# Performance work log

Hardware: AMD Instinct MI355X
Metric: run time of the kernel (lower is better)

Reference implementation:

```python
import jax, jax.numpy as jnp
import numpy as np

HEADS = 16
DIM_HEAD = 64
SCALE = DIM_HEAD ** -0.5


def setup_inputs() -> dict:
    key = jax.random.key(0)
    k1, k2, k3, k4 = jax.random.split(key, 4)
    b, n, dim = 2, 2048, 1024
    inner = HEADS * DIM_HEAD  # 1024
    return {
        "x": jax.random.normal(k1, (b, n, dim), dtype=jnp.float32),
        "x1": jax.random.normal(k2, (b, n, dim), dtype=jnp.float32),
        "W_qkv": jax.random.normal(k3, (dim, inner * 3), dtype=jnp.float32) * (dim ** -0.5),
        "W_out": jax.random.normal(k4, (inner, dim), dtype=jnp.float32) * (inner ** -0.5),
        "b_out": jnp.zeros((dim,), dtype=jnp.float32),
    }


def _split_heads(t):
    b, n, hd = t.shape
    return t.reshape(b, n, HEADS, DIM_HEAD).transpose(0, 2, 1, 3)  # b h n d


def _merge_heads(t):
    b, h, n, d = t.shape
    return t.transpose(0, 2, 1, 3).reshape(b, n, h * d)


def reference(x, x1, W_qkv, W_out, b_out):
    qkv = jnp.split(x @ W_qkv, 3, axis=-1)
    qkv1 = jnp.split(x1 @ W_qkv, 3, axis=-1)
    q, k, v = map(_split_heads, qkv)
    q1, k1, v1 = map(_split_heads, qkv1)

    # cross attention: x queries attend to x1 keys/values, and vice versa
    attn = jax.nn.softmax(jnp.einsum('bhnd,bhmd->bhnm', q, k1) * SCALE, axis=-1)
    attn1 = jax.nn.softmax(jnp.einsum('bhnd,bhmd->bhnm', q1, k) * SCALE, axis=-1)
    out = _merge_heads(jnp.einsum('bhnm,bhmd->bhnd', attn, v1))
    out1 = _merge_heads(jnp.einsum('bhnm,bhmd->bhnd', attn1, v))

    out = out @ W_out + b_out
    out1 = out1 @ W_out + b_out
    return out, out1
```

## Files before the change

kernel.cpp:

```cpp
#include <hip/hip_runtime.h>
#include <hip/hip_bf16.h>


typedef __attribute__((ext_vector_type(8))) short short8;
typedef __attribute__((ext_vector_type(4))) float f32x4;

#define MFMA_BF16(a, b, c) __builtin_amdgcn_mfma_f32_16x16x32_bf16((a), (b), (c), 0, 0, 0)

__device__ __forceinline__ ushort f2bf(float f) {
    __hip_bfloat16 h = __float2bfloat16(f);
    return *reinterpret_cast<ushort*>(&h);
}

__device__ __forceinline__ void gload_lds16(const void* g, void* l) {
    __builtin_amdgcn_global_load_lds(
        (const __attribute__((address_space(1))) void*)g,
        (__attribute__((address_space(3))) void*)l, 16, 0, 0);
}

__global__ __launch_bounds__(256) void cvt_k(const float* __restrict__ in,
                                             ushort* __restrict__ out, int n) {
    const int i = (blockIdx.x * 256 + threadIdx.x) * 4;
    if (i >= n) return;
    float4 v = *(const float4*)(in + i);
    ushort4 o;
    o.x = f2bf(v.x); o.y = f2bf(v.y); o.z = f2bf(v.z); o.w = f2bf(v.w);
    *(ushort4*)(out + i) = o;
}

__global__ __launch_bounds__(256) void transpose_cvt(const float* __restrict__ in,
                                                     ushort* __restrict__ out,
                                                     int R, int C) {
    __shared__ ushort tile[32][33];
    const int c0 = blockIdx.x * 32, r0 = blockIdx.y * 32;
    const int tx = threadIdx.x, ty = threadIdx.y;
#pragma unroll
    for (int i = 0; i < 4; ++i)
        tile[ty * 4 + i][tx] = f2bf(in[(size_t)(r0 + ty * 4 + i) * C + c0 + tx]);
    __syncthreads();
#pragma unroll
    for (int i = 0; i < 4; ++i)
        out[(size_t)(c0 + ty * 4 + i) * R + r0 + tx] = tile[tx][ty * 4 + i];
}

__global__ __launch_bounds__(256) void qkv_gemm(const ushort* __restrict__ xb,
                                                const ushort* __restrict__ wt,
                                                ushort* __restrict__ qb,
                                                ushort* __restrict__ kb,
                                                ushort* __restrict__ vb) {
    __shared__ __align__(16) ushort As[128][40];
    __shared__ __align__(16) ushort Bs[128][40];

    const int n0 = blockIdx.x * 128;
    const int m0 = blockIdx.y * 128;
    const int t = threadIdx.x;
    const int lane = t & 63, w = t >> 6;
    const int wm = (w >> 1) * 64, wn = (w & 1) * 64;
    const int l16 = lane & 15, lq = lane >> 4;
    const int r = t >> 1, kc = (t & 1) * 16;

    f32x4 acc[4][4] = {};

    for (int k0 = 0; k0 < 1024; k0 += 32) {
        __syncthreads();
        {
            const ushort* p = xb + (size_t)(m0 + r) * 1024 + k0 + kc;
            short8 v0 = *(const short8*)p;
            short8 v1 = *(const short8*)(p + 8);
            *(short8*)&As[r][kc] = v0;
            *(short8*)&As[r][kc + 8] = v1;
            const ushort* q = wt + (size_t)(n0 + r) * 1024 + k0 + kc;
            short8 u0 = *(const short8*)q;
            short8 u1 = *(const short8*)(q + 8);
            *(short8*)&Bs[r][kc] = u0;
            *(short8*)&Bs[r][kc + 8] = u1;
        }
        __syncthreads();
        short8 a[4], b[4];
#pragma unroll
        for (int i = 0; i < 4; ++i) a[i] = *(const short8*)&As[wm + i * 16 + l16][lq * 8];
#pragma unroll
        for (int j = 0; j < 4; ++j) b[j] = *(const short8*)&Bs[wn + j * 16 + l16][lq * 8];
#pragma unroll
        for (int i = 0; i < 4; ++i)
#pragma unroll
            for (int j = 0; j < 4; ++j) acc[i][j] = MFMA_BF16(a[i], b[j], acc[i][j]);
    }

    const int which = (n0 >> 10);
    const float qscale = (which == 0) ? 0.125f : 1.0f;

#pragma unroll
    for (int i = 0; i < 4; ++i) {
#pragma unroll
        for (int jj = 0; jj < 4; ++jj) {
#pragma unroll
            for (int rr = 0; rr < 4; ++rr) {
                const int m = m0 + wm + i * 16 + lq * 4 + rr;
                const int nc = n0 + wn + jj * 16 + l16;
                const ushort bv = f2bf(acc[i][jj][rr] * qscale);
                const int s = m >> 12;
                const int mm = m & 4095;
                const int rem = nc & 1023;
                const int h = rem >> 6, d = rem & 63;
                const int sb = (s << 1) | (mm >> 11);
                const int pos = mm & 2047;
                const size_t bh = (size_t)(sb * 16 + h);
                if (which == 0)      qb[(bh * 2048 + pos) * 64 + d] = bv;
                else if (which == 1) kb[(bh * 2048 + pos) * 64 + d] = bv;
                else                 vb[(bh * 64 + d) * 2048 + pos] = bv;
            }
        }
    }
}

__global__ __launch_bounds__(256, 4) void attn_k(const ushort* __restrict__ qb,
                                                 const ushort* __restrict__ kb,
                                                 const ushort* __restrict__ vb,
                                                 ushort* __restrict__ ob) {
    __shared__ __align__(16) ushort Ks[2][4096];
    __shared__ __align__(16) ushort Vs[2][4096];
    __shared__ __align__(16) ushort Pt[4][1024];

    const int t = threadIdx.x, lane = t & 63, w = t >> 6;
    const int l16 = lane & 15, lq = lane >> 4;

    const int lid = blockIdx.x;
    const int xcd = lid & 7, kk = lid >> 3;
    const int qt = kk & 15;
    const int g = xcd + ((kk >> 4) << 3);
    const int h = g & 15, sb = g >> 4;
    const int s = sb >> 1, bb = sb & 1;
    const int kvsb = ((1 - s) << 1) | bb;
    const int q0 = qt * 128 + w * 32;

    const ushort* qp = qb + (size_t)(sb * 16 + h) * 2048 * 64;
    const char* kp = (const char*)(kb + (size_t)(kvsb * 16 + h) * 2048 * 64);
    const char* vp = (const char*)(vb + (size_t)(kvsb * 16 + h) * 64 * 2048);

    short8 aq[2][2];
#pragma unroll
    for (int u = 0; u < 2; ++u)
#pragma unroll
        for (int c = 0; c < 2; ++c)
            aq[u][c] = *(const short8*)(qp + (size_t)(q0 + u * 16 + l16) * 64 + c * 32 + lq * 8);

    short8 ones;
#pragma unroll
    for (int j = 0; j < 8; ++j) ones[j] = (short)0x3F80;

    f32x4 o_acc[2][4] = {};
    f32x4 l_acc[2] = {};

    const int swl = ((lane >> 3) & 7) << 4;
    auto stage = [&](int buf, int key0) {
#pragma unroll
        for (int i = 0; i < 2; ++i) {
            const int ch = w * 2 + i;
            const int off = ch * 1024 + lane * 16;
            gload_lds16(kp + (size_t)key0 * 128 + (off ^ swl),
                        (char*)&Ks[buf][0] + ch * 1024);
            const int rd = ch * 8 + (lane >> 3);
            const int cb = (lane & 7) * 16;
            gload_lds16(vp + (size_t)rd * 4096 + (size_t)key0 * 2 + (cb ^ swl),
                        (char*)&Vs[buf][0] + ch * 1024);
        }
    };

    stage(0, 0);
    __syncthreads();

    char* Pw = (char*)&Pt[w][0];

    for (int tt = 0; tt < 32; ++tt) {
        const int cur = tt & 1;
        if (tt < 31) stage(cur ^ 1, (tt + 1) * 64);

        const char* Kc = (const char*)&Ks[cur][0];
        const char* Vc = (const char*)&Vs[cur][0];

        f32x4 sc0[4] = {}, sc1[4] = {};
#pragma unroll
        for (int j = 0; j < 4; ++j) {
            const int row = j * 16 + l16;
            const int swr = (row & 7) << 4;
            short8 k0 = *(const short8*)(Kc + row * 128 + ((lq * 16) ^ swr));
            short8 k1 = *(const short8*)(Kc + row * 128 + ((64 + lq * 16) ^ swr));
            sc0[j] = MFMA_BF16(aq[0][0], k0, sc0[j]);
            sc0[j] = MFMA_BF16(aq[0][1], k1, sc0[j]);
            sc1[j] = MFMA_BF16(aq[1][0], k0, sc1[j]);
            sc1[j] = MFMA_BF16(aq[1][1], k1, sc1[j]);
        }

        short8 ap[2][2];
#pragma unroll
        for (int j = 0; j < 4; ++j)
#pragma unroll
            for (int r2 = 0; r2 < 4; ++r2) {
                const int row = lq * 4 + r2;
                *(ushort*)(Pw + row * 128 + ((j * 32 + l16 * 2) ^ ((row & 7) << 4))) =
                    f2bf(__expf(sc0[j][r2]));
            }
        asm volatile("s_waitcnt lgkmcnt(0)" ::: "memory");
        {
            const int swr = (l16 & 7) << 4;
            ap[0][0] = *(const short8*)(Pw + l16 * 128 + ((lq * 16) ^ swr));
            ap[0][1] = *(const short8*)(Pw + l16 * 128 + ((64 + lq * 16) ^ swr));
        }
        asm volatile("s_waitcnt lgkmcnt(0)" ::: "memory");
#pragma unroll
        for (int j = 0; j < 4; ++j)
#pragma unroll
            for (int r2 = 0; r2 < 4; ++r2) {
                const int row = lq * 4 + r2;
                *(ushort*)(Pw + row * 128 + ((j * 32 + l16 * 2) ^ ((row & 7) << 4))) =
                    f2bf(__expf(sc1[j][r2]));
            }
        asm volatile("s_waitcnt lgkmcnt(0)" ::: "memory");
        {
            const int swr = (l16 & 7) << 4;
            ap[1][0] = *(const short8*)(Pw + l16 * 128 + ((lq * 16) ^ swr));
            ap[1][1] = *(const short8*)(Pw + l16 * 128 + ((64 + lq * 16) ^ swr));
        }

        l_acc[0] = MFMA_BF16(ap[0][0], ones, l_acc[0]);
        l_acc[0] = MFMA_BF16(ap[0][1], ones, l_acc[0]);
        l_acc[1] = MFMA_BF16(ap[1][0], ones, l_acc[1]);
        l_acc[1] = MFMA_BF16(ap[1][1], ones, l_acc[1]);
#pragma unroll
        for (int dt = 0; dt < 4; ++dt) {
            const int row = dt * 16 + l16;
            const int swr = (row & 7) << 4;
            short8 v0 = *(const short8*)(Vc + row * 128 + ((lq * 16) ^ swr));
            short8 v1 = *(const short8*)(Vc + row * 128 + ((64 + lq * 16) ^ swr));
            o_acc[0][dt] = MFMA_BF16(ap[0][0], v0, o_acc[0][dt]);
            o_acc[0][dt] = MFMA_BF16(ap[0][1], v1, o_acc[0][dt]);
            o_acc[1][dt] = MFMA_BF16(ap[1][0], v0, o_acc[1][dt]);
            o_acc[1][dt] = MFMA_BF16(ap[1][1], v1, o_acc[1][dt]);
        }

        __syncthreads();
    }

#pragma unroll
    for (int u = 0; u < 2; ++u) {
        float inv[4];
#pragma unroll
        for (int r2 = 0; r2 < 4; ++r2) inv[r2] = 1.f / l_acc[u][r2];
#pragma unroll
        for (int dt = 0; dt < 4; ++dt)
#pragma unroll
            for (int r2 = 0; r2 < 4; ++r2)
                ob[(size_t)(sb * 2048 + q0 + u * 16 + lq * 4 + r2) * 1024 + h * 64 + dt * 16 + l16] =
                    f2bf(o_acc[u][dt][r2] * inv[r2]);
    }
}

__global__ __launch_bounds__(256) void out_gemm(const ushort* __restrict__ ob,
                                                const ushort* __restrict__ wot,
                                                const float* __restrict__ bias,
                                                float* __restrict__ out) {
    __shared__ __align__(16) ushort As[128][40];
    __shared__ __align__(16) ushort Bs[128][40];

    const int n0 = blockIdx.x * 128;
    const int m0 = blockIdx.y * 128;
    const int t = threadIdx.x;
    const int lane = t & 63, w = t >> 6;
    const int wm = (w >> 1) * 64, wn = (w & 1) * 64;
    const int l16 = lane & 15, lq = lane >> 4;
    const int r = t >> 1, kc = (t & 1) * 16;

    f32x4 acc[4][4] = {};

    for (int k0 = 0; k0 < 1024; k0 += 32) {
        __syncthreads();
        {
            const ushort* p = ob + (size_t)(m0 + r) * 1024 + k0 + kc;
            short8 v0 = *(const short8*)p;
            short8 v1 = *(const short8*)(p + 8);
            *(short8*)&As[r][kc] = v0;
            *(short8*)&As[r][kc + 8] = v1;
            const ushort* q = wot + (size_t)(n0 + r) * 1024 + k0 + kc;
            short8 u0 = *(const short8*)q;
            short8 u1 = *(const short8*)(q + 8);
            *(short8*)&Bs[r][kc] = u0;
            *(short8*)&Bs[r][kc + 8] = u1;
        }
        __syncthreads();
        short8 a[4], b[4];
#pragma unroll
        for (int i = 0; i < 4; ++i) a[i] = *(const short8*)&As[wm + i * 16 + l16][lq * 8];
#pragma unroll
        for (int j = 0; j < 4; ++j) b[j] = *(const short8*)&Bs[wn + j * 16 + l16][lq * 8];
#pragma unroll
        for (int i = 0; i < 4; ++i)
#pragma unroll
            for (int j = 0; j < 4; ++j) acc[i][j] = MFMA_BF16(a[i], b[j], acc[i][j]);
    }

    float biasf[4];
#pragma unroll
    for (int jj = 0; jj < 4; ++jj) biasf[jj] = bias[n0 + wn + jj * 16 + l16];

#pragma unroll
    for (int i = 0; i < 4; ++i)
#pragma unroll
        for (int jj = 0; jj < 4; ++jj)
#pragma unroll
            for (int rr = 0; rr < 4; ++rr) {
                const int m = m0 + wm + i * 16 + lq * 4 + rr;
                const int nc = n0 + wn + jj * 16 + l16;
                out[(size_t)m * 1024 + nc] = acc[i][jj][rr] + biasf[jj];
            }
}

extern "C" void kernel_launch(void* const* d_in, const int* in_sizes, int n_in,
                              void* d_out, int out_size, void* d_ws, size_t ws_size,
                              hipStream_t stream) {
    (void)out_size; (void)ws_size;
    const float *x = nullptr, *x1 = nullptr, *wqkv = nullptr, *wout = nullptr, *bias = nullptr;
    for (int i = 0; i < n_in; ++i) {
        const int sz = in_sizes[i];
        const float* p = (const float*)d_in[i];
        if (sz == 4194304)      { if (!x) x = p; else x1 = p; }
        else if (sz == 3145728) wqkv = p;
        else if (sz == 1048576) wout = p;
        else if (sz == 1024)    bias = p;
    }
    float* out = (float*)d_out;

    ushort* ws      = (ushort*)d_ws;
    ushort* wqkv_t  = ws;
    ushort* wout_t  = wqkv_t + 3072 * 1024;
    ushort* xb      = wout_t + 1024 * 1024;
    ushort* qbuf    = xb + 8388608;
    ushort* kbuf    = qbuf + 8388608;
    ushort* vbuf    = kbuf + 8388608;
    ushort* obuf    = xb;

    cvt_k<<<4096, 256, 0, stream>>>(x,  xb,           4194304);
    cvt_k<<<4096, 256, 0, stream>>>(x1, xb + 4194304, 4194304);
    transpose_cvt<<<dim3(96, 32), dim3(32, 8), 0, stream>>>(wqkv, wqkv_t, 1024, 3072);
    transpose_cvt<<<dim3(32, 32), dim3(32, 8), 0, stream>>>(wout, wout_t, 1024, 1024);
    qkv_gemm<<<dim3(24, 64), 256, 0, stream>>>(xb, wqkv_t, qbuf, kbuf, vbuf);
    attn_k<<<1024, 256, 0, stream>>>(qbuf, kbuf, vbuf, obuf);
    out_gemm<<<dim3(8, 64), 256, 0, stream>>>(obuf, wout_t, bias, out);
}
```

Measured before the change: 320.8 us.

## Use direct global-to-LDS loads with XOR swizzle and BK=64 in GEMMs

Both projection GEMMs now stage A and B tiles through global_load_lds 16-byte transfers into an XOR-swizzled LDS layout, and the K step doubles to 64. The goal is to skip the register round-trip for tile staging, avoid LDS bank conflicts, and halve the number of barriers per K sweep. The two input conversion launches are also merged into one kernel. In exchange, LDS use per block grows and there is still no double buffering, so load latency stays exposed between the barriers.

After: 306.6 us. 4.5% less time.

```diff
diff --git a/kernel.cpp b/kernel.cpp
--- a/kernel.cpp
+++ b/kernel.cpp
@@ -18,14 +18,17 @@
         (__attribute__((address_space(3))) void*)l, 16, 0, 0);
 }
 
-__global__ __launch_bounds__(256) void cvt_k(const float* __restrict__ in,
-                                             ushort* __restrict__ out, int n) {
-    const int i = (blockIdx.x * 256 + threadIdx.x) * 4;
-    if (i >= n) return;
-    float4 v = *(const float4*)(in + i);
+__global__ __launch_bounds__(256) void cvt2_k(const float* __restrict__ a,
+                                              const float* __restrict__ b,
+                                              ushort* __restrict__ out) {
+    const int idx = blockIdx.x * 256 + threadIdx.x;
+    const int half = 1048576;
+    const float* src = (idx < half) ? a : b;
+    const int i = (idx < half ? idx : idx - half) * 4;
+    float4 v = *(const float4*)(src + i);
     ushort4 o;
     o.x = f2bf(v.x); o.y = f2bf(v.y); o.z = f2bf(v.z); o.w = f2bf(v.w);
-    *(ushort4*)(out + i) = o;
+    *(ushort4*)(out + (size_t)idx * 4) = o;
 }
 
 __global__ __launch_bounds__(256) void transpose_cvt(const float* __restrict__ in,
@@ -48,8 +51,8 @@
                                                 ushort* __restrict__ qb,
                                                 ushort* __restrict__ kb,
                                                 ushort* __restrict__ vb) {
-    __shared__ __align__(16) ushort As[128][40];
-    __shared__ __align__(16) ushort Bs[128][40];
+    __shared__ __align__(16) ushort As[128 * 64];
+    __shared__ __align__(16) ushort Bs[128 * 64];
 
     const int n0 = blockIdx.x * 128;
     const int m0 = blockIdx.y * 128;
@@ -57,34 +60,44 @@
     const int lane = t & 63, w = t >> 6;
     const int wm = (w >> 1) * 64, wn = (w & 1) * 64;
     const int l16 = lane & 15, lq = lane >> 4;
-    const int r = t >> 1, kc = (t & 1) * 16;
+
+    const int srow = lane >> 3;
+    const int scol = ((lane & 7) * 16) ^ (srow << 4);
 
     f32x4 acc[4][4] = {};
 
-    for (int k0 = 0; k0 < 1024; k0 += 32) {
-        __syncthreads();
-        {
-            const ushort* p = xb + (size_t)(m0 + r) * 1024 + k0 + kc;
-            short8 v0 = *(const short8*)p;
-            short8 v1 = *(const short8*)(p + 8);
-            *(short8*)&As[r][kc] = v0;
-            *(short8*)&As[r][kc + 8] = v1;
-            const ushort* q = wt + (size_t)(n0 + r) * 1024 + k0 + kc;
-            short8 u0 = *(const short8*)q;
-            short8 u1 = *(const short8*)(q + 8);
-            *(short8*)&Bs[r][kc] = u0;
-            *(short8*)&Bs[r][kc + 8] = u1;
-        }
-        __syncthreads();
-        short8 a[4], b[4];
-#pragma unroll
-        for (int i = 0; i < 4; ++i) a[i] = *(const short8*)&As[wm + i * 16 + l16][lq * 8];
-#pragma unroll
-        for (int j = 0; j < 4; ++j) b[j] = *(const short8*)&Bs[wn + j * 16 + l16][lq * 8];
-#pragma unroll
-        for (int i = 0; i < 4; ++i)
-#pragma unroll
-            for (int j = 0; j < 4; ++j) acc[i][j] = MFMA_BF16(a[i], b[j], acc[i][j]);
+    for (int k0 = 0; k0 < 1024; k0 += 64) {
+        __syncthreads();
+#pragma unroll
+        for (int c = 0; c < 4; ++c) {
+            const int ch = w * 4 + c;
+            const int row = ch * 8 + srow;
+            gload_lds16((const char*)xb + ((size_t)(m0 + row) * 1024 + k0) * 2 + scol,
+                        (char*)As + ch * 1024);
+            gload_lds16((const char*)wt + ((size_t)(n0 + row) * 1024 + k0) * 2 + scol,
+                        (char*)Bs + ch * 1024);
+        }
+        __syncthreads();
+#pragma unroll
+        for (int kc = 0; kc < 2; ++kc) {
+            short8 a[4], b[4];
+#pragma unroll
+            for (int i = 0; i < 4; ++i) {
+                const int row = wm + i * 16 + l16;
+                a[i] = *(const short8*)((const char*)As + row * 128 +
+                                        ((kc * 64 + lq * 16) ^ ((row & 7) << 4)));
+            }
+#pragma unroll
+            for (int j = 0; j < 4; ++j) {
+                const int row = wn + j * 16 + l16;
+                b[j] = *(const short8*)((const char*)Bs + row * 128 +
+                                        ((kc * 64 + lq * 16) ^ ((row & 7) << 4)));
+            }
+#pragma unroll
+            for (int i = 0; i < 4; ++i)
+#pragma unroll
+                for (int j = 0; j < 4; ++j) acc[i][j] = MFMA_BF16(a[i], b[j], acc[i][j]);
+        }
     }
 
     const int which = (n0 >> 10);
@@ -260,8 +273,8 @@
                                                 const ushort* __restrict__ wot,
                                                 const float* __restrict__ bias,
                                                 float* __restrict__ out) {
-    __shared__ __align__(16) ushort As[128][40];
-    __shared__ __align__(16) ushort Bs[128][40];
+    __shared__ __align__(16) ushort As[128 * 64];
+    __shared__ __align__(16) ushort Bs[128 * 64];
 
     const int n0 = blockIdx.x * 128;
     const int m0 = blockIdx.y * 128;
@@ -269,34 +282,44 @@
     const int lane = t & 63, w = t >> 6;
     const int wm = (w >> 1) * 64, wn = (w & 1) * 64;
     const int l16 = lane & 15, lq = lane >> 4;
-    const int r = t >> 1, kc = (t & 1) * 16;
+
+    const int srow = lane >> 3;
+    const int scol = ((lane & 7) * 16) ^ (srow << 4);
 
     f32x4 acc[4][4] = {};
 
-    for (int k0 = 0; k0 < 1024; k0 += 32) {
-        __syncthreads();
-        {
-            const ushort* p = ob + (size_t)(m0 + r) * 1024 + k0 + kc;
-            short8 v0 = *(const short8*)p;
-            short8 v1 = *(const short8*)(p + 8);
-            *(short8*)&As[r][kc] = v0;
-            *(short8*)&As[r][kc + 8] = v1;
-            const ushort* q = wot + (size_t)(n0 + r) * 1024 + k0 + kc;
-            short8 u0 = *(const short8*)q;
-            short8 u1 = *(const short8*)(q + 8);
-            *(short8*)&Bs[r][kc] = u0;
-            *(short8*)&Bs[r][kc + 8] = u1;
-        }
-        __syncthreads();
-        short8 a[4], b[4];
-#pragma unroll
-        for (int i = 0; i < 4; ++i) a[i] = *(const short8*)&As[wm + i * 16 + l16][lq * 8];
-#pragma unroll
-        for (int j = 0; j < 4; ++j) b[j] = *(const short8*)&Bs[wn + j * 16 + l16][lq * 8];
-#pragma unroll
-        for (int i = 0; i < 4; ++i)
-#pragma unroll
-            for (int j = 0; j < 4; ++j) acc[i][j] = MFMA_BF16(a[i], b[j], acc[i][j]);
+    for (int k0 = 0; k0 < 1024; k0 += 64) {
+        __syncthreads();
+#pragma unroll
+        for (int c = 0; c < 4; ++c) {
+            const int ch = w * 4 + c;
+            const int row = ch * 8 + srow;
+            gload_lds16((const char*)ob + ((size_t)(m0 + row) * 1024 + k0) * 2 + scol,
+                        (char*)As + ch * 1024);
+            gload_lds16((const char*)wot + ((size_t)(n0 + row) * 1024 + k0) * 2 + scol,
+                        (char*)Bs + ch * 1024);
+        }
+        __syncthreads();
+#pragma unroll
+        for (int kc = 0; kc < 2; ++kc) {
+            short8 a[4], b[4];
+#pragma unroll
+            for (int i = 0; i < 4; ++i) {
+                const int row = wm + i * 16 + l16;
+                a[i] = *(const short8*)((const char*)As + row * 128 +
+                                        ((kc * 64 + lq * 16) ^ ((row & 7) << 4)));
+            }
+#pragma unroll
+            for (int j = 0; j < 4; ++j) {
+                const int row = wn + j * 16 + l16;
+                b[j] = *(const short8*)((const char*)Bs + row * 128 +
+                                        ((kc * 64 + lq * 16) ^ ((row & 7) << 4)));
+            }
+#pragma unroll
+            for (int i = 0; i < 4; ++i)
+#pragma unroll
+                for (int j = 0; j < 4; ++j) acc[i][j] = MFMA_BF16(a[i], b[j], acc[i][j]);
+        }
     }
 
     float biasf[4];
@@ -339,8 +362,7 @@
     ushort* vbuf    = kbuf + 8388608;
     ushort* obuf    = xb;
 
-    cvt_k<<<4096, 256, 0, stream>>>(x,  xb,           4194304);
-    cvt_k<<<4096, 256, 0, stream>>>(x1, xb + 4194304, 4194304);
+    cvt2_k<<<8192, 256, 0, stream>>>(x, x1, xb);
     transpose_cvt<<<dim3(96, 32), dim3(32, 8), 0, stream>>>(wqkv, wqkv_t, 1024, 3072);
     transpose_cvt<<<dim3(32, 32), dim3(32, 8), 0, stream>>>(wout, wout_t, 1024, 1024);
     qkv_gemm<<<dim3(24, 64), 256, 0, stream>>>(xb, wqkv_t, qbuf, kbuf, vbuf);
```
